# Performance work log

Measured on AMD Instinct MI355X. Metric: run time of the kernel, lower is better.

The kernel has to match this reference:

```python
import jax, jax.numpy as jnp
import numpy as np

PI = np.pi

def rgb_to_lab(img):
    # img: [B,3,H,W] sRGB in [0,1]. Matches kornia.color.rgb_to_lab.
    lin = jnp.where(img > 0.04045, jnp.power((img + 0.055) / 1.055, 2.4), img / 12.92)
    r, g, b = lin[:, 0], lin[:, 1], lin[:, 2]
    x = 0.412453 * r + 0.357580 * g + 0.180423 * b
    y = 0.212671 * r + 0.715160 * g + 0.072169 * b
    z = 0.019334 * r + 0.119193 * g + 0.950227 * b
    # normalize by D65 white point
    xn = x / 0.95047
    yn = y
    zn = z / 1.08883
    def f(t):
        return jnp.where(t > 0.008856, jnp.power(jnp.maximum(t, 1e-8), 1.0 / 3.0), 7.787 * t + 4.0 / 29.0)
    fx, fy, fz = f(xn), f(yn), f(zn)
    L = 116.0 * fy - 16.0
    a = 500.0 * (fx - fy)
    bb = 200.0 * (fy - fz)
    return L, a, bb  # each [B,H,W]

def deltaE_ciede2000(L1, a1, b1, L2, a2, b2):
    # skimage.color.deltaE_ciede2000 with kL=kC=kH=1
    C1 = jnp.hypot(a1, b1)
    C2 = jnp.hypot(a2, b2)
    Cbar = 0.5 * (C1 + C2)
    c7 = Cbar ** 7
    G = 0.5 * (1.0 - jnp.sqrt(c7 / (c7 + 25.0 ** 7)))
    scale = 1.0 + G
    a1p = a1 * scale
    a2p = a2 * scale
    C1p = jnp.hypot(a1p, b1)
    C2p = jnp.hypot(a2p, b2)
    h1 = jnp.arctan2(b1, a1p); h1 = jnp.where(h1 < 0, h1 + 2 * PI, h1)
    h2 = jnp.arctan2(b2, a2p); h2 = jnp.where(h2 < 0, h2 + 2 * PI, h2)
    # lightness term
    Lbar = 0.5 * (L1 + L2)
    tmp = (Lbar - 50.0) ** 2
    SL = 1.0 + 0.015 * tmp / jnp.sqrt(20.0 + tmp)
    L_term = (L2 - L1) / SL
    # chroma term
    Cbarp = 0.5 * (C1p + C2p)
    SC = 1.0 + 0.045 * Cbarp
    C_term = (C2p - C1p) / SC
    # hue term
    h_diff = h2 - h1
    h_sum = h1 + h2
    CC = C1p * C2p
    dH = jnp.where(h_diff > PI, h_diff - 2 * PI, jnp.where(h_diff < -PI, h_diff + 2 * PI, h_diff))
    dH = jnp.where(CC == 0.0, 0.0, dH)
    dH_term = 2.0 * jnp.sqrt(CC) * jnp.sin(dH / 2.0)
    mask = (CC != 0.0) & (jnp.abs(h_diff) > PI)
    Hbar = jnp.where(mask & (h_sum < 2 * PI), h_sum + 2 * PI,
                     jnp.where(mask & (h_sum >= 2 * PI), h_sum - 2 * PI, h_sum))
    Hbar = jnp.where(CC == 0.0, h_sum * 2.0, Hbar)
    Hbar = 0.5 * Hbar
    T = (1.0 - 0.17 * jnp.cos(Hbar - PI / 6.0)
         + 0.24 * jnp.cos(2.0 * Hbar)
         + 0.32 * jnp.cos(3.0 * Hbar + PI / 30.0)
         - 0.20 * jnp.cos(4.0 * Hbar - 63.0 * PI / 180.0))
    SH = 1.0 + 0.015 * Cbarp * T
    H_term = dH_term / SH
    # rotation term
    c7p = Cbarp ** 7
    Rc = 2.0 * jnp.sqrt(c7p / (c7p + 25.0 ** 7))
    dtheta = (PI / 6.0) * jnp.exp(-(((Hbar * 180.0 / PI) - 275.0) / 25.0) ** 2)
    R_term = -jnp.sin(2.0 * dtheta) * Rc * C_term * H_term
    dE2 = L_term ** 2 + C_term ** 2 + H_term ** 2 + R_term
    return jnp.sqrt(jnp.maximum(dE2, 0.0))


def setup_inputs() -> dict:
    key = jax.random.key(0)
    k1, k2 = jax.random.split(key)
    img1 = jax.random.uniform(k1, (16, 3, 512, 512), dtype=jnp.float32)
    img2 = jax.random.uniform(k2, (16, 3, 512, 512), dtype=jnp.float32)
    return {"img1": img1, "img2": img2}


def reference(img1, img2):
    L1, a1, b1 = rgb_to_lab(img1)
    L2, a2, b2 = rgb_to_lab(img2)
    delE = deltaE_ciede2000(L1, a1, b1, L2, a2, b2)  # [B,H,W]
    return delE / 100.0
```

## Files before the change

### kernel.cpp

```cpp
#include <hip/hip_runtime.h>
#include <math.h>

#define PI_F      3.14159265358979323846f
#define TWO_PI_F  6.28318530717958647692f
#define INV_2PI_F 0.15915494309189533577f

typedef float v2 __attribute__((ext_vector_type(2)));

__device__ __forceinline__ float fsqrt(float x)  { return __builtin_amdgcn_sqrtf(x); }
__device__ __forceinline__ float frcp(float x)   { return __builtin_amdgcn_rcpf(x); }
__device__ __forceinline__ float frsq(float x)   { return __builtin_amdgcn_rsqf(x); }
__device__ __forceinline__ float fexp2(float x)  { return __builtin_amdgcn_exp2f(x); }
__device__ __forceinline__ float flog2(float x)  { return __builtin_amdgcn_logf(x); }
__device__ __forceinline__ float fsin(float x)   { return __builtin_amdgcn_sinf(x * INV_2PI_F); }
__device__ __forceinline__ float fcos(float x)   { return __builtin_amdgcn_cosf(x * INV_2PI_F); }

__device__ __forceinline__ v2 V(float s){ v2 r; r.x = s; r.y = s; return r; }
#if __has_builtin(__builtin_elementwise_fma)
__device__ __forceinline__ v2 vfma(v2 a, v2 b, v2 c){ return __builtin_elementwise_fma(a, b, c); }
#else
__device__ __forceinline__ v2 vfma(v2 a, v2 b, v2 c){ v2 r; r.x=__fmaf_rn(a.x,b.x,c.x); r.y=__fmaf_rn(a.y,b.y,c.y); return r; }
#endif
__device__ __forceinline__ v2 vmax0(v2 a){ v2 r; r.x=fmaxf(a.x,0.0f); r.y=fmaxf(a.y,0.0f); return r; }
__device__ __forceinline__ v2 vsqrt(v2 x){ v2 r; r.x=fsqrt(x.x); r.y=fsqrt(x.y); return r; }
__device__ __forceinline__ v2 vrcp (v2 x){ v2 r; r.x=frcp(x.x);  r.y=frcp(x.y);  return r; }
__device__ __forceinline__ v2 vrsq (v2 x){ v2 r; r.x=frsq(x.x);  r.y=frsq(x.y);  return r; }
__device__ __forceinline__ v2 vexp2(v2 x){ v2 r; r.x=fexp2(x.x); r.y=fexp2(x.y); return r; }
__device__ __forceinline__ v2 vsinr(v2 x){ v2 r; r.x=fsin(x.x); r.y=fsin(x.y); return r; }
__device__ __forceinline__ v2 vcosr(v2 x){ v2 r; r.x=fcos(x.x); r.y=fcos(x.y); return r; }


__device__ __forceinline__ float fast_atan2(float y, float x) {
    float ax = fabsf(x), ay = fabsf(y);
    float mx = fmaxf(ax, ay), mn = fminf(ax, ay);
    float r = mn * frcp(mx);
    float s = r * r;
    float p = __fmaf_rn(s, -0.01172120f, 0.05265332f);
    p = __fmaf_rn(s, p, -0.11643287f);
    p = __fmaf_rn(s, p,  0.19354346f);
    p = __fmaf_rn(s, p, -0.33262347f);
    p = __fmaf_rn(s, p,  0.99997726f);
    float th = r * p;
    th = (ay > ax)   ? (1.57079632679f - th) : th;
    th = (x < 0.0f)  ? (PI_F - th)           : th;
    th = (y < 0.0f)  ? -th                   : th;
    th = (mx == 0.0f) ? 0.0f : th;
    return th;
}

__device__ __forceinline__ float srgb_lin(float c) {
    float u = __fmaf_rn(c, 1.0f / 1.055f, 0.055f / 1.055f);
    float p = fexp2(2.4f * flog2(u));
    float l = c * (1.0f / 12.92f);
    return (c > 0.04045f) ? p : l;
}

__device__ __forceinline__ float labf(float t) {
    float cr = fexp2(0.333333333333f * flog2(t));
    float ln = __fmaf_rn(7.787f, t, 4.0f / 29.0f);
    return (t > 0.008856f) ? cr : ln;
}

__device__ __forceinline__ void rgb2lab(float r, float g, float b,
                                        float& L, float& A, float& B) {
    r = srgb_lin(r); g = srgb_lin(g); b = srgb_lin(b);
    float xn = 0.4339463f * r + 0.3762135f * g + 0.1898252f * b;
    float yn = 0.212671f  * r + 0.71516f   * g + 0.072169f  * b;
    float zn = 0.0177566f * r + 0.1094694f * g + 0.8727056f * b;
    float fx = labf(xn);
    float fy = labf(yn);
    float fz = labf(zn);
    L = __fmaf_rn(116.0f, fy, -16.0f);
    A = 500.0f * (fx - fy);
    B = 200.0f * (fy - fz);
}

__device__ __forceinline__ void upstream_px(float r1, float g1, float bl1,
                                            float r2, float g2, float bl2,
                                            float& L1o, float& L2o,
                                            float& C1po, float& C2po,
                                            float& dHto, float& Hbo) {
    float L1, A1, B1, L2, A2, B2;
    rgb2lab(r1, g1, bl1, L1, A1, B1);
    rgb2lab(r2, g2, bl2, L2, A2, B2);

    const float P25_7 = 6103515625.0f;

    float C1 = fsqrt(__fmaf_rn(A1, A1, B1 * B1));
    float C2 = fsqrt(__fmaf_rn(A2, A2, B2 * B2));
    float Cbar = 0.5f * (C1 + C2);
    float cb2 = Cbar * Cbar;
    float c7 = cb2 * cb2 * cb2 * Cbar;
    float G = __fmaf_rn(-0.5f * c7, frsq(__fmaf_rn(c7, c7, __fmaf_rn(P25_7, c7, 1e-20f))), 0.5f);
    float s = 1.0f + G;
    float a1p = A1 * s, a2p = A2 * s;
    float C1p = fsqrt(__fmaf_rn(a1p, a1p, B1 * B1));
    float C2p = fsqrt(__fmaf_rn(a2p, a2p, B2 * B2));

    float h1 = fast_atan2(B1, a1p); h1 = (h1 < 0.0f) ? h1 + TWO_PI_F : h1;
    float h2 = fast_atan2(B2, a2p); h2 = (h2 < 0.0f) ? h2 + TWO_PI_F : h2;

    float h_diff = h2 - h1;
    float h_sum  = h1 + h2;
    float CC = C1p * C2p;
    bool cc0 = (CC == 0.0f);

    float dH = (h_diff > PI_F) ? (h_diff - TWO_PI_F)
             : ((h_diff < -PI_F) ? (h_diff + TWO_PI_F) : h_diff);
    if (cc0) dH = 0.0f;
    float dH_term = 2.0f * fsqrt(CC) * fsin(0.5f * dH);

    bool mask = (!cc0) && (fabsf(h_diff) > PI_F);
    float Hbar = h_sum;
    if (mask) Hbar = (h_sum < TWO_PI_F) ? (h_sum + TWO_PI_F) : (h_sum - TWO_PI_F);
    if (cc0)  Hbar = h_sum * 2.0f;
    Hbar *= 0.5f;

    L1o = L1; L2o = L2; C1po = C1p; C2po = C2p; dHto = dH_term; Hbo = Hbar;
}


__global__ __launch_bounds__(64) void ciede_kernel(
    const float* __restrict__ img1, const float* __restrict__ img2,
    float* __restrict__ out, int n2_total) {
    int idx = blockIdx.x * 64 + threadIdx.x;
    if (idx >= n2_total) return;

    const int PLANE2 = 131072;
    int n = idx >> 17;
    int j = idx & (PLANE2 - 1);

    const float2* p1 = reinterpret_cast<const float2*>(img1) + (size_t)n * 3 * PLANE2;
    const float2* p2 = reinterpret_cast<const float2*>(img2) + (size_t)n * 3 * PLANE2;

    float2 r1 = p1[j], g1 = p1[j + PLANE2], b1 = p1[j + 2 * PLANE2];
    float2 r2 = p2[j], g2 = p2[j + PLANE2], b2 = p2[j + 2 * PLANE2];

    const float P25_7 = 6103515625.0f;

    v2 L1, L2, C1p, C2p, dHt, Hb;
    {
        float a, b, c, d, e, f;
        upstream_px(r1.x, g1.x, b1.x, r2.x, g2.x, b2.x, a, b, c, d, e, f);
        L1.x = a; L2.x = b; C1p.x = c; C2p.x = d; dHt.x = e; Hb.x = f;
        upstream_px(r1.y, g1.y, b1.y, r2.y, g2.y, b2.y, a, b, c, d, e, f);
        L1.y = a; L2.y = b; C1p.y = c; C2p.y = d; dHt.y = e; Hb.y = f;
    }

    v2 Lbar = (L1 + L2) * 0.5f;
    v2 lt = Lbar - V(50.0f);
    v2 tmp = lt * lt;
    v2 SL = vfma(tmp * 0.015f, vrsq(V(20.0f) + tmp), V(1.0f));

    v2 Cbarp = (C1p + C2p) * 0.5f;
    v2 SC = vfma(V(0.045f), Cbarp, V(1.0f));

    v2 ch = vcosr(Hb);
    v2 sh = vsinr(Hb);
    v2 c2 = vfma(ch * 2.0f, ch, V(-1.0f));
    v2 s2 = sh * ch * 2.0f;
    v2 c3 = ch * c2 - sh * s2;
    v2 s3 = sh * c2 + ch * s2;
    v2 c4 = vfma(c2 * 2.0f, c2, V(-1.0f));
    v2 s4 = s2 * c2 * 2.0f;
    v2 T1 = vfma(ch, V(0.86602540378f), sh * 0.5f);
    v2 T3 = vfma(c3, V(0.99452189536f), s3 * -0.10452846327f);
    v2 T4 = vfma(c4, V(0.45399049974f), s4 * 0.89100652419f);
    v2 T = V(1.0f) - T1 * 0.17f + c2 * 0.24f + T3 * 0.32f - T4 * 0.20f;
    v2 SH = vfma(Cbarp * 0.015f, T, V(1.0f));

    v2 PQ  = SC * SH;
    v2 inv = vrcp(SL * PQ);
    v2 L_term = (L2 - L1) * PQ * inv;
    v2 C_term = (C2p - C1p) * (SL * SH) * inv;
    v2 H_term = dHt * (SL * SC) * inv;

    v2 cp2 = Cbarp * Cbarp;
    v2 c7p = cp2 * cp2 * cp2 * Cbarp;
    v2 Rc = c7p * 2.0f * vrsq(vfma(c7p, c7p, vfma(V(P25_7), c7p, V(1e-20f))));

    v2 hd = vfma(Hb, V(2.752769787f), V(-13.2123465f));
    v2 vv = vexp2(-(hd * hd)) * 1.04719755119f;
    v2 w  = vv * vv;
    v2 sp = vfma(w, V(-1.0f / 5040.0f), V(1.0f / 120.0f));
    sp = vfma(w, sp, V(-1.0f / 6.0f));
    sp = vfma(w, sp, V(1.0f));
    v2 sin2dt = vv * sp;
    v2 R_term = -(sin2dt * Rc * C_term * H_term);

    v2 dE2 = vfma(L_term, L_term, vfma(C_term, C_term, vfma(H_term, H_term, R_term)));
    v2 o = vsqrt(vmax0(dE2)) * 0.01f;

    float2 ov; ov.x = o.x; ov.y = o.y;
    reinterpret_cast<float2*>(out)[idx] = ov;
}

extern "C" void kernel_launch(void* const* d_in, const int* in_sizes, int n_in,
                              void* d_out, int out_size, void* d_ws, size_t ws_size,
                              hipStream_t stream) {
    const float* img1 = (const float*)d_in[0];
    const float* img2 = (const float*)d_in[1];
    float* out = (float*)d_out;

    int n2 = out_size / 2;
    int grid = (n2 + 63) / 64;
    ciede_kernel<<<grid, 64, 0, stream>>>(img1, img2, out, n2);
}
```

Before: 126.3 us.

## Process four pixels per thread with float4 loads and packed v2 upstream math

Each thread now handles four pixels using float4 loads and stores instead of two with float2, and the block size grows from 64 to 256. The Lab conversion, chroma and atan2 stages are rewritten on two-wide vectors so the compiler can emit packed FP32 instructions. The goal is more instruction-level parallelism, fewer memory instructions and less per-pixel scalar ALU work. The cost is higher register pressure, which may lower occupancy.

Measured after the change: 128.6 us. No clear change (+1.9%).

```diff
diff --git a/kernel.cpp b/kernel.cpp
--- a/kernel.cpp
+++ b/kernel.cpp
@@ -16,6 +16,7 @@
 __device__ __forceinline__ float fcos(float x)   { return __builtin_amdgcn_cosf(x * INV_2PI_F); }
 
 __device__ __forceinline__ v2 V(float s){ v2 r; r.x = s; r.y = s; return r; }
+__device__ __forceinline__ v2 V2(float a, float b){ v2 r; r.x = a; r.y = b; return r; }
 #if __has_builtin(__builtin_elementwise_fma)
 __device__ __forceinline__ v2 vfma(v2 a, v2 b, v2 c){ return __builtin_elementwise_fma(a, b, c); }
 #else
@@ -30,76 +31,65 @@
 __device__ __forceinline__ v2 vcosr(v2 x){ v2 r; r.x=fcos(x.x); r.y=fcos(x.y); return r; }
 
 
-__device__ __forceinline__ float fast_atan2(float y, float x) {
-    float ax = fabsf(x), ay = fabsf(y);
-    float mx = fmaxf(ax, ay), mn = fminf(ax, ay);
-    float r = mn * frcp(mx);
-    float s = r * r;
-    float p = __fmaf_rn(s, -0.01172120f, 0.05265332f);
-    p = __fmaf_rn(s, p, -0.11643287f);
-    p = __fmaf_rn(s, p,  0.19354346f);
-    p = __fmaf_rn(s, p, -0.33262347f);
-    p = __fmaf_rn(s, p,  0.99997726f);
-    float th = r * p;
-    th = (ay > ax)   ? (1.57079632679f - th) : th;
-    th = (x < 0.0f)  ? (PI_F - th)           : th;
-    th = (y < 0.0f)  ? -th                   : th;
-    th = (mx == 0.0f) ? 0.0f : th;
+__device__ __forceinline__ v2 vatan2(v2 y, v2 x) {
+    v2 ax, ay; ax.x = fabsf(x.x); ax.y = fabsf(x.y); ay.x = fabsf(y.x); ay.y = fabsf(y.y);
+    v2 mx, mn;
+    mx.x = fmaxf(ax.x, ay.x); mx.y = fmaxf(ax.y, ay.y);
+    mn.x = fminf(ax.x, ay.x); mn.y = fminf(ax.y, ay.y);
+    v2 r = mn * vrcp(mx);
+    v2 s = r * r;
+    v2 p = vfma(s, V(-0.01172120f), V(0.05265332f));
+    p = vfma(s, p, V(-0.11643287f));
+    p = vfma(s, p, V( 0.19354346f));
+    p = vfma(s, p, V(-0.33262347f));
+    p = vfma(s, p, V( 0.99997726f));
+    v2 th = r * p;
+    th.x = (ay.x > ax.x)   ? (1.57079632679f - th.x) : th.x;
+    th.y = (ay.y > ax.y)   ? (1.57079632679f - th.y) : th.y;
+    th.x = (x.x < 0.0f)    ? (PI_F - th.x)           : th.x;
+    th.y = (x.y < 0.0f)    ? (PI_F - th.y)           : th.y;
+    th.x = (y.x < 0.0f)    ? -th.x                   : th.x;
+    th.y = (y.y < 0.0f)    ? -th.y                   : th.y;
+    th.x = (mx.x == 0.0f)  ? 0.0f                    : th.x;
+    th.y = (mx.y == 0.0f)  ? 0.0f                    : th.y;
     return th;
 }
 
-__device__ __forceinline__ float srgb_lin(float c) {
-    float u = __fmaf_rn(c, 1.0f / 1.055f, 0.055f / 1.055f);
-    float p = fexp2(2.4f * flog2(u));
-    float l = c * (1.0f / 12.92f);
-    return (c > 0.04045f) ? p : l;
-}
-
-__device__ __forceinline__ float labf(float t) {
-    float cr = fexp2(0.333333333333f * flog2(t));
-    float ln = __fmaf_rn(7.787f, t, 4.0f / 29.0f);
-    return (t > 0.008856f) ? cr : ln;
-}
-
-__device__ __forceinline__ void rgb2lab(float r, float g, float b,
-                                        float& L, float& A, float& B) {
-    r = srgb_lin(r); g = srgb_lin(g); b = srgb_lin(b);
-    float xn = 0.4339463f * r + 0.3762135f * g + 0.1898252f * b;
-    float yn = 0.212671f  * r + 0.71516f   * g + 0.072169f  * b;
-    float zn = 0.0177566f * r + 0.1094694f * g + 0.8727056f * b;
-    float fx = labf(xn);
-    float fy = labf(yn);
-    float fz = labf(zn);
-    L = __fmaf_rn(116.0f, fy, -16.0f);
+__device__ __forceinline__ v2 vsrgb_lin(v2 c) {
+    v2 u = vfma(c, V(1.0f / 1.055f), V(0.055f / 1.055f));
+    v2 p; p.x = fexp2(2.4f * flog2(u.x)); p.y = fexp2(2.4f * flog2(u.y));
+    v2 l = c * (1.0f / 12.92f);
+    v2 r;
+    r.x = (c.x > 0.04045f) ? p.x : l.x;
+    r.y = (c.y > 0.04045f) ? p.y : l.y;
+    return r;
+}
+
+__device__ __forceinline__ v2 vlabf(v2 t) {
+    v2 cr; cr.x = fexp2(0.333333333333f * flog2(t.x)); cr.y = fexp2(0.333333333333f * flog2(t.y));
+    v2 ln = vfma(V(7.787f), t, V(4.0f / 29.0f));
+    v2 r;
+    r.x = (t.x > 0.008856f) ? cr.x : ln.x;
+    r.y = (t.y > 0.008856f) ? cr.y : ln.y;
+    return r;
+}
+
+__device__ __forceinline__ void vrgb2lab(v2 r, v2 g, v2 b,
+                                         v2& L, v2& A, v2& B) {
+    r = vsrgb_lin(r); g = vsrgb_lin(g); b = vsrgb_lin(b);
+    v2 xn = 0.4339463f * r + 0.3762135f * g + 0.1898252f * b;
+    v2 yn = 0.212671f  * r + 0.71516f   * g + 0.072169f  * b;
+    v2 zn = 0.0177566f * r + 0.1094694f * g + 0.8727056f * b;
+    v2 fx = vlabf(xn);
+    v2 fy = vlabf(yn);
+    v2 fz = vlabf(zn);
+    L = vfma(V(116.0f), fy, V(-16.0f));
     A = 500.0f * (fx - fy);
     B = 200.0f * (fy - fz);
 }
 
-__device__ __forceinline__ void upstream_px(float r1, float g1, float bl1,
-                                            float r2, float g2, float bl2,
-                                            float& L1o, float& L2o,
-                                            float& C1po, float& C2po,
-                                            float& dHto, float& Hbo) {
-    float L1, A1, B1, L2, A2, B2;
-    rgb2lab(r1, g1, bl1, L1, A1, B1);
-    rgb2lab(r2, g2, bl2, L2, A2, B2);
-
-    const float P25_7 = 6103515625.0f;
-
-    float C1 = fsqrt(__fmaf_rn(A1, A1, B1 * B1));
-    float C2 = fsqrt(__fmaf_rn(A2, A2, B2 * B2));
-    float Cbar = 0.5f * (C1 + C2);
-    float cb2 = Cbar * Cbar;
-    float c7 = cb2 * cb2 * cb2 * Cbar;
-    float G = __fmaf_rn(-0.5f * c7, frsq(__fmaf_rn(c7, c7, __fmaf_rn(P25_7, c7, 1e-20f))), 0.5f);
-    float s = 1.0f + G;
-    float a1p = A1 * s, a2p = A2 * s;
-    float C1p = fsqrt(__fmaf_rn(a1p, a1p, B1 * B1));
-    float C2p = fsqrt(__fmaf_rn(a2p, a2p, B2 * B2));
-
-    float h1 = fast_atan2(B1, a1p); h1 = (h1 < 0.0f) ? h1 + TWO_PI_F : h1;
-    float h2 = fast_atan2(B2, a2p); h2 = (h2 < 0.0f) ? h2 + TWO_PI_F : h2;
-
+__device__ __forceinline__ void hue_tail(float h1, float h2, float C1p, float C2p,
+                                         float& dHt, float& Hb) {
     float h_diff = h2 - h1;
     float h_sum  = h1 + h2;
     float CC = C1p * C2p;
@@ -108,44 +98,59 @@
     float dH = (h_diff > PI_F) ? (h_diff - TWO_PI_F)
              : ((h_diff < -PI_F) ? (h_diff + TWO_PI_F) : h_diff);
     if (cc0) dH = 0.0f;
-    float dH_term = 2.0f * fsqrt(CC) * fsin(0.5f * dH);
+    dHt = 2.0f * fsqrt(CC) * fsin(0.5f * dH);
 
     bool mask = (!cc0) && (fabsf(h_diff) > PI_F);
     float Hbar = h_sum;
     if (mask) Hbar = (h_sum < TWO_PI_F) ? (h_sum + TWO_PI_F) : (h_sum - TWO_PI_F);
     if (cc0)  Hbar = h_sum * 2.0f;
-    Hbar *= 0.5f;
-
-    L1o = L1; L2o = L2; C1po = C1p; C2po = C2p; dHto = dH_term; Hbo = Hbar;
-}
-
-
-__global__ __launch_bounds__(64) void ciede_kernel(
-    const float* __restrict__ img1, const float* __restrict__ img2,
-    float* __restrict__ out, int n2_total) {
-    int idx = blockIdx.x * 64 + threadIdx.x;
-    if (idx >= n2_total) return;
-
-    const int PLANE2 = 131072;
-    int n = idx >> 17;
-    int j = idx & (PLANE2 - 1);
-
-    const float2* p1 = reinterpret_cast<const float2*>(img1) + (size_t)n * 3 * PLANE2;
-    const float2* p2 = reinterpret_cast<const float2*>(img2) + (size_t)n * 3 * PLANE2;
-
-    float2 r1 = p1[j], g1 = p1[j + PLANE2], b1 = p1[j + 2 * PLANE2];
-    float2 r2 = p2[j], g2 = p2[j + PLANE2], b2 = p2[j + 2 * PLANE2];
+    Hb = 0.5f * Hbar;
+}
+
+__device__ __forceinline__ void upstream_v2(v2 r1, v2 g1, v2 bl1,
+                                            v2 r2, v2 g2, v2 bl2,
+                                            v2& L1o, v2& L2o,
+                                            v2& C1po, v2& C2po,
+                                            v2& dHto, v2& Hbo) {
+    v2 L1, A1, B1, L2, A2, B2;
+    vrgb2lab(r1, g1, bl1, L1, A1, B1);
+    vrgb2lab(r2, g2, bl2, L2, A2, B2);
 
     const float P25_7 = 6103515625.0f;
 
-    v2 L1, L2, C1p, C2p, dHt, Hb;
+    v2 C1 = vsqrt(vfma(A1, A1, B1 * B1));
+    v2 C2 = vsqrt(vfma(A2, A2, B2 * B2));
+    v2 Cbar = 0.5f * (C1 + C2);
+    v2 cb2 = Cbar * Cbar;
+    v2 c7 = cb2 * cb2 * cb2 * Cbar;
+    v2 G = vfma(-0.5f * c7, vrsq(vfma(c7, c7, vfma(V(P25_7), c7, V(1e-20f)))), V(0.5f));
+    v2 s = V(1.0f) + G;
+    v2 a1p = A1 * s, a2p = A2 * s;
+    v2 C1p = vsqrt(vfma(a1p, a1p, B1 * B1));
+    v2 C2p = vsqrt(vfma(a2p, a2p, B2 * B2));
+
+    v2 h1 = vatan2(B1, a1p);
+    h1.x = (h1.x < 0.0f) ? h1.x + TWO_PI_F : h1.x;
+    h1.y = (h1.y < 0.0f) ? h1.y + TWO_PI_F : h1.y;
+    v2 h2 = vatan2(B2, a2p);
+    h2.x = (h2.x < 0.0f) ? h2.x + TWO_PI_F : h2.x;
+    h2.y = (h2.y < 0.0f) ? h2.y + TWO_PI_F : h2.y;
+
+    v2 dHt, Hb;
     {
-        float a, b, c, d, e, f;
-        upstream_px(r1.x, g1.x, b1.x, r2.x, g2.x, b2.x, a, b, c, d, e, f);
-        L1.x = a; L2.x = b; C1p.x = c; C2p.x = d; dHt.x = e; Hb.x = f;
-        upstream_px(r1.y, g1.y, b1.y, r2.y, g2.y, b2.y, a, b, c, d, e, f);
-        L1.y = a; L2.y = b; C1p.y = c; C2p.y = d; dHt.y = e; Hb.y = f;
+        float d0, b0, d1, b1v;
+        hue_tail(h1.x, h2.x, C1p.x, C2p.x, d0, b0);
+        hue_tail(h1.y, h2.y, C1p.y, C2p.y, d1, b1v);
+        dHt.x = d0; dHt.y = d1; Hb.x = b0; Hb.y = b1v;
     }
+
+    L1o = L1; L2o = L2; C1po = C1p; C2po = C2p; dHto = dHt; Hbo = Hb;
+}
+
+
+__device__ __forceinline__ v2 downstream_v2(v2 L1, v2 L2, v2 C1p, v2 C2p,
+                                            v2 dHt, v2 Hb) {
+    const float P25_7 = 6103515625.0f;
 
     v2 Lbar = (L1 + L2) * 0.5f;
     v2 lt = Lbar - V(50.0f);
@@ -189,10 +194,41 @@
     v2 R_term = -(sin2dt * Rc * C_term * H_term);
 
     v2 dE2 = vfma(L_term, L_term, vfma(C_term, C_term, vfma(H_term, H_term, R_term)));
-    v2 o = vsqrt(vmax0(dE2)) * 0.01f;
-
-    float2 ov; ov.x = o.x; ov.y = o.y;
-    reinterpret_cast<float2*>(out)[idx] = ov;
+    return vsqrt(vmax0(dE2)) * 0.01f;
+}
+
+
+__global__ __launch_bounds__(256) void ciede_kernel(
+    const float* __restrict__ img1, const float* __restrict__ img2,
+    float* __restrict__ out, int n4_total) {
+    int idx = blockIdx.x * 256 + threadIdx.x;
+    if (idx >= n4_total) return;
+
+    const int PLANE4 = 65536;
+    int n = idx >> 16;
+    int j = idx & (PLANE4 - 1);
+
+    const float4* p1 = reinterpret_cast<const float4*>(img1) + (size_t)n * 3 * PLANE4;
+    const float4* p2 = reinterpret_cast<const float4*>(img2) + (size_t)n * 3 * PLANE4;
+
+    float4 R1 = p1[j], G1 = p1[j + PLANE4], B1 = p1[j + 2 * PLANE4];
+    float4 R2 = p2[j], G2 = p2[j + PLANE4], B2 = p2[j + 2 * PLANE4];
+
+    v2 L1a, L2a, C1pa, C2pa, dHta, Hba;
+    v2 L1b, L2b, C1pb, C2pb, dHtb, Hbb;
+    upstream_v2(V2(R1.x, R1.y), V2(G1.x, G1.y), V2(B1.x, B1.y),
+                V2(R2.x, R2.y), V2(G2.x, G2.y), V2(B2.x, B2.y),
+                L1a, L2a, C1pa, C2pa, dHta, Hba);
+    upstream_v2(V2(R1.z, R1.w), V2(G1.z, G1.w), V2(B1.z, B1.w),
+                V2(R2.z, R2.w), V2(G2.z, G2.w), V2(B2.z, B2.w),
+                L1b, L2b, C1pb, C2pb, dHtb, Hbb);
+
+    v2 oa = downstream_v2(L1a, L2a, C1pa, C2pa, dHta, Hba);
+    v2 ob = downstream_v2(L1b, L2b, C1pb, C2pb, dHtb, Hbb);
+
+    float4 o4;
+    o4.x = oa.x; o4.y = oa.y; o4.z = ob.x; o4.w = ob.y;
+    reinterpret_cast<float4*>(out)[idx] = o4;
 }
 
 extern "C" void kernel_launch(void* const* d_in, const int* in_sizes, int n_in,
@@ -202,7 +238,7 @@
     const float* img2 = (const float*)d_in[1];
     float* out = (float*)d_out;
 
-    int n2 = out_size / 2;
-    int grid = (n2 + 63) / 64;
-    ciede_kernel<<<grid, 64, 0, stream>>>(img1, img2, out, n2);
-}
+    int n4 = out_size / 4;
+    int grid = (n4 + 255) / 256;
+    ciede_kernel<<<grid, 256, 0, stream>>>(img1, img2, out, n4);
+}
```
